# Kernel optimization log

Hardware: AMD Instinct MI355X
Metric: run time of the kernel (lower is better)

## Reference

```python
import jax, jax.numpy as jnp
import numpy as np

# dims
B, CIN, H, W = 64, 96, 28, 28
E = 4            # num_experts
EXPAND = 6
HID = CIN * EXPAND   # 576
K = 5
STRIDE = 1
PAD = K // 2
RED = max(1, int(CIN * 0.25))      # SE reduced dim = 24
RHID = max(16, CIN // 4)           # routing hidden = 24
COUT = 96
EPS = 1e-3


def setup_inputs() -> dict:
    key = jax.random.key(0)
    ks = jax.random.split(key, 12)
    rn = lambda k, shape, s=0.05: jax.random.normal(k, shape, jnp.float32) * s
    return dict(
        x=jax.random.normal(ks[0], (B, CIN, H, W), jnp.float32),
        # routing net: Linear(CIN->RHID) + ReLU + Linear(RHID->E)
        r_w1=rn(ks[1], (RHID, CIN)), r_b1=jnp.zeros((RHID,), jnp.float32),
        r_w2=rn(ks[2], (E, RHID)), r_b2=jnp.zeros((E,), jnp.float32),
        # expand 1x1 conv (no bias)
        exp_w=rn(ks[3], (HID, CIN)),
        bn1_g=jnp.ones((HID,), jnp.float32), bn1_b=jnp.zeros((HID,), jnp.float32),
        bn1_m=jnp.zeros((HID,), jnp.float32), bn1_v=jnp.ones((HID,), jnp.float32),
        # MoE depthwise expert kernels [E, HID, K, K]
        dw_w=rn(ks[4], (E, HID, K, K)),
        bn2_g=jnp.ones((HID,), jnp.float32), bn2_b=jnp.zeros((HID,), jnp.float32),
        bn2_m=jnp.zeros((HID,), jnp.float32), bn2_v=jnp.ones((HID,), jnp.float32),
        # squeeze-excitation 1x1 convs (with bias)
        se_w1=rn(ks[5], (RED, HID)), se_b1=jnp.zeros((RED,), jnp.float32),
        se_w2=rn(ks[6], (HID, RED)), se_b2=jnp.zeros((HID,), jnp.float32),
        # MoE pointwise expert kernels [E, COUT, HID]
        pw_w=rn(ks[7], (E, COUT, HID)),
        bn3_g=jnp.ones((COUT,), jnp.float32), bn3_b=jnp.zeros((COUT,), jnp.float32),
        bn3_m=jnp.zeros((COUT,), jnp.float32), bn3_v=jnp.ones((COUT,), jnp.float32),
    )


def _bn(y, g, b, m, v):
    sh = (1, -1, 1, 1)
    inv = g.reshape(sh) * jax.lax.rsqrt(v.reshape(sh) + EPS)
    return (y - m.reshape(sh)) * inv + b.reshape(sh)


def _dwconv_per_sample(x, kernels):
    # x [b,c,h,w], kernels [b,c,k,k] -> per-sample depthwise conv
    c = x.shape[1]
    def one(xi, wi):
        return jax.lax.conv_general_dilated(
            xi[None], wi[:, None],  # [1,c,h,w], [c,1,k,k]
            window_strides=(STRIDE, STRIDE),
            padding=[(PAD, PAD), (PAD, PAD)],
            feature_group_count=c,
            dimension_numbers=('NCHW', 'OIHW', 'NCHW'))[0]
    return jax.vmap(one)(x, kernels)


def reference(x, r_w1, r_b1, r_w2, r_b2, exp_w,
              bn1_g, bn1_b, bn1_m, bn1_v, dw_w,
              bn2_g, bn2_b, bn2_m, bn2_v,
              se_w1, se_b1, se_w2, se_b2, pw_w,
              bn3_g, bn3_b, bn3_m, bn3_v):
    silu = jax.nn.silu
    # routing: global avg pool -> MLP -> softmax (temperature = 1.0)
    pool = x.mean(axis=(2, 3))                          # [b, cin]
    hdn = jax.nn.relu(pool @ r_w1.T + r_b1)             # [b, rhid]
    logits = (hdn @ r_w2.T + r_b2).astype(jnp.float32)  # [b, E]
    rw = jax.nn.softmax(logits, axis=-1).astype(x.dtype)
    # expand 1x1 conv + BN + SiLU
    out = jnp.einsum('oc,bchw->bohw', exp_w, x)         # [b, hid, h, w]
    out = silu(_bn(out, bn1_g, bn1_b, bn1_m, bn1_v))
    # MoE depthwise: aggregate per-sample kernels, per-sample depthwise conv
    kern = jnp.einsum('be,eckl->bckl', rw, dw_w)        # [b, hid, k, k]
    out = _dwconv_per_sample(out, kern)
    out = silu(_bn(out, bn2_g, bn2_b, bn2_m, bn2_v))
    # squeeze-excitation
    s = out.mean(axis=(2, 3))                           # [b, hid]
    z = silu(s @ se_w1.T + se_b1)                       # [b, red]
    sc = jax.nn.sigmoid(z @ se_w2.T + se_b2)            # [b, hid]
    out = out * sc[:, :, None, None]
    # MoE pointwise projection: per-sample 1x1 conv weights
    wpw = jnp.einsum('be,eoc->boc', rw, pw_w)           # [b, cout, hid]
    out = jnp.einsum('boc,bchw->bohw', wpw, out)        # [b, cout, h, w]
    out = _bn(out, bn3_g, bn3_b, bn3_m, bn3_v)
    # residual (stride==1, cin==cout); stochastic depth is identity in eval
    return x + out
```

## Files before the change

kernel.cpp:

```cpp
#include <hip/hip_runtime.h>
#include <hip/hip_bf16.h>
#include <math.h>

#define B 64
#define CIN 96
#define HH 28
#define WW 28
#define NPIX 784
#define E 4
#define HID 576
#define RED 24
#define RHID 24
#define COUT 96
#define EPS 1e-3f

typedef __attribute__((ext_vector_type(8))) short short8v;
typedef __attribute__((ext_vector_type(4))) float f32x4;

__device__ __forceinline__ float sigmoidf_(float v) { return 1.0f / (1.0f + __expf(-v)); }

__device__ __forceinline__ unsigned short f2bf(float v) {
    __hip_bfloat16 h = __float2bfloat16(v);
    return *reinterpret_cast<unsigned short*>(&h);
}

__device__ __forceinline__ float bf2f(unsigned short u) {
    unsigned int w = ((unsigned int)u) << 16;
    return *reinterpret_cast<float*>(&w);
}

__global__ __launch_bounds__(256) void k_pool(const float* __restrict__ x, float* __restrict__ pool) {
    int row = blockIdx.x * 4 + (threadIdx.x >> 6);
    int lane = threadIdx.x & 63;
    const float4* xr = reinterpret_cast<const float4*>(x + (size_t)row * NPIX);
    float s = 0.f;
    for (int i = lane; i < 196; i += 64) {
        float4 v = xr[i];
        s += v.x + v.y + v.z + v.w;
    }
#pragma unroll
    for (int off = 32; off > 0; off >>= 1) s += __shfl_down(s, off);
    if (lane == 0) pool[row] = s * (1.0f / NPIX);
}

__global__ __launch_bounds__(256) void k_mlp(const float* __restrict__ pool,
                                             const float* __restrict__ r_w1, const float* __restrict__ r_b1,
                                             const float* __restrict__ r_w2, const float* __restrict__ r_b2,
                                             float* __restrict__ rw) {
    __shared__ float w1[RHID * CIN];
    __shared__ float b1s[RHID];
    __shared__ float w2[E * RHID];
    __shared__ float b2s[E];
    __shared__ float pl[B * CIN];
    int tid = threadIdx.x;
    for (int i = tid; i < RHID * CIN; i += 256) w1[i] = r_w1[i];
    if (tid < RHID) b1s[tid] = r_b1[tid];
    if (tid < E * RHID) w2[tid] = r_w2[tid];
    if (tid < E) b2s[tid] = r_b2[tid];
    for (int i = tid; i < B * CIN; i += 256) pl[i] = pool[i];
    __syncthreads();
    if (tid < B) {
        const float* p = pl + tid * CIN;
        float hdn[RHID];
#pragma unroll
        for (int r = 0; r < RHID; ++r) {
            float a = b1s[r];
            for (int c = 0; c < CIN; ++c) a += p[c] * w1[r * CIN + c];
            hdn[r] = fmaxf(a, 0.f);
        }
        float lg[E];
        float mx = -1e30f;
#pragma unroll
        for (int e = 0; e < E; ++e) {
            float a = b2s[e];
#pragma unroll
            for (int r = 0; r < RHID; ++r) a += hdn[r] * w2[e * RHID + r];
            lg[e] = a;
            mx = fmaxf(mx, a);
        }
        float den = 0.f;
#pragma unroll
        for (int e = 0; e < E; ++e) { lg[e] = __expf(lg[e] - mx); den += lg[e]; }
#pragma unroll
        for (int e = 0; e < E; ++e) rw[tid * E + e] = lg[e] / den;
    }
}

__global__ void k_wcvt(const float* __restrict__ w, unsigned short* __restrict__ wb) {
    int i = blockIdx.x * blockDim.x + threadIdx.x;
    if (i < HID * CIN) wb[i] = f2bf(w[i]);
}

__global__ __launch_bounds__(256) void k_expand_mfma(
    const float* __restrict__ x, const unsigned short* __restrict__ w_bf,
    const float* __restrict__ bn1_g, const float* __restrict__ bn1_b,
    const float* __restrict__ bn1_m, const float* __restrict__ bn1_v,
    __hip_bfloat16* __restrict__ hid) {
    int nc = blockIdx.x;
    int b = blockIdx.y;
    int tid = threadIdx.x;
    int lane = tid & 63, wv = tid >> 6;
    int col = lane & 15, g = lane >> 4;
    __shared__ unsigned short xt[96 * 116];
    __shared__ float inv1s[HID], sh1s[HID];

    for (int i = tid; i < HID; i += 256) {
        float inv = bn1_g[i] * rsqrtf(bn1_v[i] + EPS);
        inv1s[i] = inv;
        sh1s[i] = bn1_b[i] - bn1_m[i] * inv;
    }
    const float* xb = x + (size_t)b * CIN * NPIX + nc * 112;
    for (int i = tid; i < 96 * 28; i += 256) {
        int c = i / 28, q = i % 28;
        float4 v = *reinterpret_cast<const float4*>(&xb[c * NPIX + q * 4]);
        ushort4 s;
        s.x = f2bf(v.x); s.y = f2bf(v.y); s.z = f2bf(v.z); s.w = f2bf(v.w);
        *reinterpret_cast<ushort4*>(&xt[c * 116 + q * 4]) = s;
    }
    __syncthreads();

    const short8v* wv8 = reinterpret_cast<const short8v*>(w_bf);
    for (int nf = 0; nf < 7; ++nf) {
        int pcol = nf * 16 + col;
        short8v bfr[3];
#pragma unroll
        for (int kk = 0; kk < 3; ++kk) {
            int k0 = kk * 32 + 8 * g;
#pragma unroll
            for (int j = 0; j < 8; ++j) bfr[kk][j] = (short)xt[(k0 + j) * 116 + pcol];
        }
        int px = nc * 112 + pcol;
#pragma unroll
        for (int mi = 0; mi < 9; ++mi) {
            int mb = (wv * 9 + mi) * 16;
            f32x4 acc = {0.f, 0.f, 0.f, 0.f};
#pragma unroll
            for (int kk = 0; kk < 3; ++kk) {
                short8v af = wv8[((mb + col) * 96 + kk * 32 + 8 * g) >> 3];
                acc = __builtin_amdgcn_mfma_f32_16x16x32_bf16(af, bfr[kk], acc, 0, 0, 0);
            }
#pragma unroll
            for (int r = 0; r < 4; ++r) {
                int oc = mb + 4 * g + r;
                float t = acc[r] * inv1s[oc] + sh1s[oc];
                float u = t * sigmoidf_(t);
                hid[((size_t)b * HID + oc) * NPIX + px] = __float2bfloat16(u);
            }
        }
    }
}

#define CT 16
#define RSF 33
#define PCSF 1063
__global__ __launch_bounds__(448) void k_dw(
    __hip_bfloat16* __restrict__ hid, const float* __restrict__ rw,
    const float* __restrict__ dw_w,
    const float* __restrict__ bn2_g, const float* __restrict__ bn2_b,
    const float* __restrict__ bn2_m, const float* __restrict__ bn2_v,
    float* __restrict__ s_out) {
    int ct = blockIdx.x;
    int b = blockIdx.y;
    int tid = threadIdx.x;
    int cb = ct * CT;
    __shared__ float PF[CT * PCSF];
    __shared__ float kl[CT][25];
    __shared__ float ssum[CT];
    __hip_bfloat16* hb = hid + ((size_t)b * HID + cb) * NPIX;

    for (int i = tid; i < CT * PCSF; i += 448) PF[i] = 0.f;
    if (tid < CT) ssum[tid] = 0.f;
    __syncthreads();

    int ci = tid / 28, w = tid - ci * 28;
    {
        const unsigned int* src = reinterpret_cast<const unsigned int*>(hb) + ci * (NPIX / 2) + w * 14;
        float* dst = PF + ci * PCSF + (w + 2) * RSF + 2;
#pragma unroll
        for (int d = 0; d < 14; ++d) {
            unsigned int v = src[d];
            dst[2 * d]     = bf2f((unsigned short)(v & 0xffffu));
            dst[2 * d + 1] = bf2f((unsigned short)(v >> 16));
        }
    }
    {
        float rwl[E];
#pragma unroll
        for (int e = 0; e < E; ++e) rwl[e] = rw[b * E + e];
        for (int i = tid; i < CT * 25; i += 448) {
            int c2 = i / 25, j = i % 25;
            int c = cb + c2;
            float a = 0.f;
#pragma unroll
            for (int e = 0; e < E; ++e) a += rwl[e] * dw_w[((size_t)e * HID + c) * 25 + j];
            kl[c2][j] = a * (bn2_g[c] * rsqrtf(bn2_v[c] + EPS));
        }
    }
    __syncthreads();

    const float* Pc = PF + ci * PCSF + w;
    float k[25];
#pragma unroll
    for (int j = 0; j < 25; ++j) k[j] = kl[ci][j];
    int c = cb + ci;
    float inv2 = bn2_g[c] * rsqrtf(bn2_v[c] + EPS);
    float sh2 = bn2_b[c] - bn2_m[c] * inv2;
    unsigned short* hout = reinterpret_cast<unsigned short*>(hb) + ci * NPIX + w;

    float win[5][5];
#pragma unroll
    for (int i = 0; i < 5; ++i)
#pragma unroll
        for (int j = 0; j < 5; ++j) win[i][j] = Pc[i * RSF + j];

    float csum = 0.f;
#pragma unroll
    for (int h = 0; h < HH; ++h) {
        float o = 0.f;
#pragma unroll
        for (int i = 0; i < 5; ++i)
#pragma unroll
            for (int j = 0; j < 5; ++j) o += win[i][j] * k[i * 5 + j];
        float t = o + sh2;
        float u = t * sigmoidf_(t);
        csum += u;
        hout[h * WW] = f2bf(u);
        if (h < HH - 1) {
#pragma unroll
            for (int i = 0; i < 4; ++i)
#pragma unroll
                for (int j = 0; j < 5; ++j) win[i][j] = win[i + 1][j];
#pragma unroll
            for (int j = 0; j < 5; ++j) win[4][j] = Pc[(h + 5) * RSF + j];
        }
    }
    atomicAdd(&ssum[ci], csum);
    __syncthreads();
    if (tid < CT) s_out[(size_t)b * HID + cb + tid] = ssum[tid] * (1.0f / NPIX);
}

__global__ __launch_bounds__(256) void k_se_wpw(
    const float* __restrict__ s, const float* __restrict__ se_w1,
    const float* __restrict__ se_b1, const float* __restrict__ se_w2,
    const float* __restrict__ se_b2, const float* __restrict__ rw,
    const float* __restrict__ pw_w,
    const float* __restrict__ bn3_g, const float* __restrict__ bn3_v,
    unsigned short* __restrict__ wpw) {
    int seg = blockIdx.x;
    int b = blockIdx.y;
    int tid = threadIdx.x;
    __shared__ float sl[HID];
    __shared__ float zl[RED];
    __shared__ float scl[HID];
    for (int i = tid; i < HID; i += 256) sl[i] = s[(size_t)b * HID + i];
    __syncthreads();
    if (tid < RED) {
        float a = se_b1[tid];
        for (int c = 0; c < HID; ++c) a += sl[c] * se_w1[tid * HID + c];
        zl[tid] = a * sigmoidf_(a);
    }
    __syncthreads();
    for (int c = tid; c < HID; c += 256) {
        float a = se_b2[c];
#pragma unroll
        for (int r = 0; r < RED; ++r) a += zl[r] * se_w2[c * RED + r];
        scl[c] = sigmoidf_(a);
    }
    __syncthreads();
    float rwl[E];
#pragma unroll
    for (int e = 0; e < E; ++e) rwl[e] = rw[b * E + e];
    unsigned short* wb = wpw + (size_t)b * COUT * HID;
    for (int i = tid; i < 16 * HID; i += 256) {
        int o = seg * 16 + i / HID, c = i % HID;
        float a = 0.f;
#pragma unroll
        for (int e = 0; e < E; ++e) a += rwl[e] * pw_w[((size_t)e * COUT + o) * HID + c];
        float inv3 = bn3_g[o] * rsqrtf(bn3_v[o] + EPS);
        wb[o * HID + c] = f2bf(a * inv3 * scl[c]);
    }
}

__global__ __launch_bounds__(448) void k_pw_mfma(
    const __hip_bfloat16* __restrict__ hid, const unsigned short* __restrict__ wpw,
    const float* __restrict__ x,
    const float* __restrict__ bn3_g, const float* __restrict__ bn3_b,
    const float* __restrict__ bn3_m, const float* __restrict__ bn3_v,
    float* __restrict__ out) {
    int nc = blockIdx.x;
    int b = blockIdx.y;
    int tid = threadIdx.x;
    int lane = tid & 63, nf = tid >> 6;
    int col = lane & 15, g = lane >> 4;
    __shared__ unsigned short Wl[96 * 104];
    __shared__ unsigned short Ht[96 * 116];
    __shared__ float inv3s[COUT], sh3s[COUT];
    if (tid < COUT) {
        float inv = bn3_g[tid] * rsqrtf(bn3_v[tid] + EPS);
        inv3s[tid] = inv;
        sh3s[tid] = bn3_b[tid] - bn3_m[tid] * inv;
    }
    const unsigned short* hb = (const unsigned short*)hid + (size_t)b * HID * NPIX + nc * 112;
    const unsigned short* wb = wpw + (size_t)b * COUT * HID;
    f32x4 acc[6];
#pragma unroll
    for (int m = 0; m < 6; ++m) acc[m] = (f32x4){0.f, 0.f, 0.f, 0.f};

    for (int ks = 0; ks < 6; ++ks) {
        __syncthreads();
        for (int i = tid; i < 96 * 48; i += 448) {
            int m = i / 48, k2 = i % 48;
            *(uint*)&Wl[m * 104 + 2 * k2] = *(const uint*)&wb[m * HID + ks * 96 + 2 * k2];
        }
        for (int i = tid; i < 96 * 56; i += 448) {
            int k = i / 56, p2 = i % 56;
            *(uint*)&Ht[k * 116 + 2 * p2] = *(const uint*)&hb[((size_t)(ks * 96 + k)) * NPIX + 2 * p2];
        }
        __syncthreads();
#pragma unroll
        for (int kk = 0; kk < 3; ++kk) {
            int k0 = kk * 32 + 8 * g;
            short8v bfr;
#pragma unroll
            for (int j = 0; j < 8; ++j) bfr[j] = (short)Ht[(k0 + j) * 116 + nf * 16 + col];
#pragma unroll
            for (int m = 0; m < 6; ++m) {
                short8v af = *(const short8v*)&Wl[(m * 16 + col) * 104 + kk * 32 + 8 * g];
                acc[m] = __builtin_amdgcn_mfma_f32_16x16x32_bf16(af, bfr, acc[m], 0, 0, 0);
            }
        }
    }
    int px = nc * 112 + nf * 16 + col;
#pragma unroll
    for (int m = 0; m < 6; ++m) {
#pragma unroll
        for (int r = 0; r < 4; ++r) {
            int oc = m * 16 + 4 * g + r;
            size_t off = ((size_t)b * COUT + oc) * NPIX + px;
            out[off] = acc[m][r] + sh3s[oc] + x[off];
        }
    }
}

extern "C" void kernel_launch(void* const* d_in, const int* in_sizes, int n_in,
                              void* d_out, int out_size, void* d_ws, size_t ws_size,
                              hipStream_t stream) {
    const float* x     = (const float*)d_in[0];
    const float* r_w1  = (const float*)d_in[1];
    const float* r_b1  = (const float*)d_in[2];
    const float* r_w2  = (const float*)d_in[3];
    const float* r_b2  = (const float*)d_in[4];
    const float* exp_w = (const float*)d_in[5];
    const float* bn1_g = (const float*)d_in[6];
    const float* bn1_b = (const float*)d_in[7];
    const float* bn1_m = (const float*)d_in[8];
    const float* bn1_v = (const float*)d_in[9];
    const float* dw_w  = (const float*)d_in[10];
    const float* bn2_g = (const float*)d_in[11];
    const float* bn2_b = (const float*)d_in[12];
    const float* bn2_m = (const float*)d_in[13];
    const float* bn2_v = (const float*)d_in[14];
    const float* se_w1 = (const float*)d_in[15];
    const float* se_b1 = (const float*)d_in[16];
    const float* se_w2 = (const float*)d_in[17];
    const float* se_b2 = (const float*)d_in[18];
    const float* pw_w  = (const float*)d_in[19];
    const float* bn3_g = (const float*)d_in[20];
    const float* bn3_b = (const float*)d_in[21];
    const float* bn3_m = (const float*)d_in[22];
    const float* bn3_v = (const float*)d_in[23];
    float* out = (float*)d_out;

    char* ws = (char*)d_ws;
    float* rw                 = (float*)(ws + 0);
    float* pool               = (float*)(ws + 1024);
    float* s                  = (float*)(ws + 26624);
    unsigned short* exp_w_bf  = (unsigned short*)(ws + 174336);
    unsigned short* wpw_bf    = (unsigned short*)(ws + 285184);
    __hip_bfloat16* hid       = (__hip_bfloat16*)(ws + 7363328);

    k_pool<<<B * CIN / 4, 256, 0, stream>>>(x, pool);
    k_mlp<<<1, 256, 0, stream>>>(pool, r_w1, r_b1, r_w2, r_b2, rw);
    k_wcvt<<<(HID * CIN + 255) / 256, 256, 0, stream>>>(exp_w, exp_w_bf);
    k_expand_mfma<<<dim3(7, B), 256, 0, stream>>>(x, exp_w_bf, bn1_g, bn1_b, bn1_m, bn1_v, hid);
    k_dw<<<dim3(36, B), 448, 0, stream>>>(hid, rw, dw_w, bn2_g, bn2_b, bn2_m, bn2_v, s);
    k_se_wpw<<<dim3(6, B), 256, 0, stream>>>(s, se_w1, se_b1, se_w2, se_b2, rw, pw_w, bn3_g, bn3_v, wpw_bf);
    k_pw_mfma<<<dim3(7, B), 448, 0, stream>>>(hid, wpw_bf, x, bn3_g, bn3_b, bn3_m, bn3_v, out);
}
```

Measured before the change: 324.7 us.

## Fuse pool with weight conversion, hoist expand A-fragments, parallelize SE, widen loads

Merges the weight bf16 conversion into the pooling kernel, saving one launch. The expand kernel now loads its weight fragments into registers once, before the barrier, instead of re-reading them for every pixel tile. The SE first layer is split across 8 lanes per output with a shuffle reduction, and the pointwise kernel's shared-memory staging uses wider vector loads. Holding all the A fragments in registers adds a lot of register pressure and could lower occupancy.

```diff
diff --git a/kernel.cpp b/kernel.cpp
--- a/kernel.cpp
+++ b/kernel.cpp
@@ -29,18 +29,24 @@
     return *reinterpret_cast<float*>(&w);
 }
 
-__global__ __launch_bounds__(256) void k_pool(const float* __restrict__ x, float* __restrict__ pool) {
-    int row = blockIdx.x * 4 + (threadIdx.x >> 6);
-    int lane = threadIdx.x & 63;
-    const float4* xr = reinterpret_cast<const float4*>(x + (size_t)row * NPIX);
-    float s = 0.f;
-    for (int i = lane; i < 196; i += 64) {
-        float4 v = xr[i];
-        s += v.x + v.y + v.z + v.w;
-    }
-#pragma unroll
-    for (int off = 32; off > 0; off >>= 1) s += __shfl_down(s, off);
-    if (lane == 0) pool[row] = s * (1.0f / NPIX);
+__global__ __launch_bounds__(256) void k_pool_wcvt(const float* __restrict__ x, float* __restrict__ pool,
+                                                   const float* __restrict__ w, unsigned short* __restrict__ wb) {
+    if (blockIdx.x < 1536) {
+        int row = blockIdx.x * 4 + (threadIdx.x >> 6);
+        int lane = threadIdx.x & 63;
+        const float4* xr = reinterpret_cast<const float4*>(x + (size_t)row * NPIX);
+        float s = 0.f;
+        for (int i = lane; i < 196; i += 64) {
+            float4 v = xr[i];
+            s += v.x + v.y + v.z + v.w;
+        }
+#pragma unroll
+        for (int off = 32; off > 0; off >>= 1) s += __shfl_down(s, off);
+        if (lane == 0) pool[row] = s * (1.0f / NPIX);
+    } else {
+        int i = (blockIdx.x - 1536) * 256 + threadIdx.x;
+        wb[i] = f2bf(w[i]);
+    }
 }
 
 __global__ __launch_bounds__(256) void k_mlp(const float* __restrict__ pool,
@@ -86,11 +92,6 @@
     }
 }
 
-__global__ void k_wcvt(const float* __restrict__ w, unsigned short* __restrict__ wb) {
-    int i = blockIdx.x * blockDim.x + threadIdx.x;
-    if (i < HID * CIN) wb[i] = f2bf(w[i]);
-}
-
 __global__ __launch_bounds__(256) void k_expand_mfma(
     const float* __restrict__ x, const unsigned short* __restrict__ w_bf,
     const float* __restrict__ bn1_g, const float* __restrict__ bn1_b,
@@ -117,9 +118,17 @@
         s.x = f2bf(v.x); s.y = f2bf(v.y); s.z = f2bf(v.z); s.w = f2bf(v.w);
         *reinterpret_cast<ushort4*>(&xt[c * 116 + q * 4]) = s;
     }
-    __syncthreads();
 
     const short8v* wv8 = reinterpret_cast<const short8v*>(w_bf);
+    short8v af[9][3];
+#pragma unroll
+    for (int mi = 0; mi < 9; ++mi) {
+#pragma unroll
+        for (int kk = 0; kk < 3; ++kk)
+            af[mi][kk] = wv8[(((wv * 9 + mi) * 16 + col) * 96 + kk * 32 + 8 * g) >> 3];
+    }
+    __syncthreads();
+
     for (int nf = 0; nf < 7; ++nf) {
         int pcol = nf * 16 + col;
         short8v bfr[3];
@@ -135,10 +144,8 @@
             int mb = (wv * 9 + mi) * 16;
             f32x4 acc = {0.f, 0.f, 0.f, 0.f};
 #pragma unroll
-            for (int kk = 0; kk < 3; ++kk) {
-                short8v af = wv8[((mb + col) * 96 + kk * 32 + 8 * g) >> 3];
-                acc = __builtin_amdgcn_mfma_f32_16x16x32_bf16(af, bfr[kk], acc, 0, 0, 0);
-            }
+            for (int kk = 0; kk < 3; ++kk)
+                acc = __builtin_amdgcn_mfma_f32_16x16x32_bf16(af[mi][kk], bfr[kk], acc, 0, 0, 0);
 #pragma unroll
             for (int r = 0; r < 4; ++r) {
                 int oc = mb + 4 * g + r;
@@ -254,10 +261,17 @@
     __shared__ float scl[HID];
     for (int i = tid; i < HID; i += 256) sl[i] = s[(size_t)b * HID + i];
     __syncthreads();
-    if (tid < RED) {
-        float a = se_b1[tid];
-        for (int c = 0; c < HID; ++c) a += sl[c] * se_w1[tid * HID + c];
-        zl[tid] = a * sigmoidf_(a);
+    if (tid < RED * 8) {
+        int r = tid >> 3, l = tid & 7;
+        float a = 0.f;
+        for (int c = l; c < HID; c += 8) a += sl[c] * se_w1[r * HID + c];
+        a += __shfl_down(a, 4, 8);
+        a += __shfl_down(a, 2, 8);
+        a += __shfl_down(a, 1, 8);
+        if (l == 0) {
+            a += se_b1[r];
+            zl[r] = a * sigmoidf_(a);
+        }
     }
     __syncthreads();
     for (int c = tid; c < HID; c += 256) {
@@ -308,13 +322,13 @@
 
     for (int ks = 0; ks < 6; ++ks) {
         __syncthreads();
-        for (int i = tid; i < 96 * 48; i += 448) {
-            int m = i / 48, k2 = i % 48;
-            *(uint*)&Wl[m * 104 + 2 * k2] = *(const uint*)&wb[m * HID + ks * 96 + 2 * k2];
-        }
-        for (int i = tid; i < 96 * 56; i += 448) {
-            int k = i / 56, p2 = i % 56;
-            *(uint*)&Ht[k * 116 + 2 * p2] = *(const uint*)&hb[((size_t)(ks * 96 + k)) * NPIX + 2 * p2];
+        for (int i = tid; i < 96 * 12; i += 448) {
+            int m = i / 12, q = i % 12;
+            *(uint4*)&Wl[m * 104 + 8 * q] = *(const uint4*)&wb[m * HID + ks * 96 + 8 * q];
+        }
+        for (int i = tid; i < 96 * 28; i += 448) {
+            int k = i / 28, q = i % 28;
+            *(uint2*)&Ht[k * 116 + 4 * q] = *(const uint2*)&hb[((size_t)(ks * 96 + k)) * NPIX + 4 * q];
         }
         __syncthreads();
 #pragma unroll
@@ -379,9 +393,8 @@
     unsigned short* wpw_bf    = (unsigned short*)(ws + 285184);
     __hip_bfloat16* hid       = (__hip_bfloat16*)(ws + 7363328);
 
-    k_pool<<<B * CIN / 4, 256, 0, stream>>>(x, pool);
+    k_pool_wcvt<<<1536 + 216, 256, 0, stream>>>(x, pool, exp_w, exp_w_bf);
     k_mlp<<<1, 256, 0, stream>>>(pool, r_w1, r_b1, r_w2, r_b2, rw);
-    k_wcvt<<<(HID * CIN + 255) / 256, 256, 0, stream>>>(exp_w, exp_w_bf);
     k_expand_mfma<<<dim3(7, B), 256, 0, stream>>>(x, exp_w_bf, bn1_g, bn1_b, bn1_m, bn1_v, hid);
     k_dw<<<dim3(36, B), 448, 0, stream>>>(hid, rw, dw_w, bn2_g, bn2_b, bn2_m, bn2_v, s);
     k_se_wpw<<<dim3(6, B), 256, 0, stream>>>(s, se_w1, se_b1, se_w2, se_b2, rw, pw_w, bn3_g, bn3_v, wpw_bf);
```

Result: faster. 295.9 us (-8.9%).
